# Optimization experiments

Hardware: AMD Instinct MI355X
Metric: run time of the kernel (lower is better)

The kernel has to match this reference:

```python
import jax, jax.numpy as jnp
import numpy as np

ORDER = 1024
U_SIZE = 128
Y_SIZE = 128
N_STEPS = 32768


def setup_inputs() -> dict:
    key = jax.random.key(0)
    k0, k1, k2, k3, k4 = jax.random.split(key, 5)
    inp = jax.random.normal(k0, (N_STEPS, U_SIZE), dtype=jnp.float32)
    # A scaled to spectral radius ~0.9 so the 32k-step recurrence is stable.
    A_w = jax.random.normal(k1, (ORDER, ORDER), dtype=jnp.float32) * (0.9 / np.sqrt(ORDER))
    B_w = jax.random.normal(k2, (ORDER, U_SIZE), dtype=jnp.float32) / np.sqrt(U_SIZE)
    C_w = jax.random.normal(k3, (Y_SIZE, ORDER), dtype=jnp.float32) / np.sqrt(ORDER)
    D_w = jax.random.normal(k4, (Y_SIZE, U_SIZE), dtype=jnp.float32) / np.sqrt(U_SIZE)
    return {"inp": inp, "A_w": A_w, "B_w": B_w, "C_w": C_w, "D_w": D_w}


def reference(inp, A_w, B_w, C_w, D_w):
    u_size = B_w.shape[1]
    order = A_w.shape[0]
    # Faithful to torch: input.reshape(u_size, -1), then column t is u at step t.
    us = inp.reshape(u_size, -1).T  # (N, u_size)
    x0 = jnp.zeros((order,), dtype=inp.dtype)

    def step(x, u):
        y = C_w @ x + D_w @ u          # (y_size,)
        x_next = A_w @ x + B_w @ u     # (order,)
        return x_next, y

    _, ys = jax.lax.scan(step, x0, us)
    return ys  # (N, y_size)
```

## Files before the change

### kernel.cpp

```cpp
#include <hip/hip_runtime.h>
#include <hip/hip_bf16.h>


#define NSTEPS 32768
#define LTRUNC 64
#define NDBLK  (LTRUNC + 1)
#define KTOT   (NDBLK * 128)
#define SPLITK 2

typedef __attribute__((ext_vector_type(8))) short short8;
typedef __attribute__((ext_vector_type(4))) float f32x4;
typedef __hip_bfloat16 bf16;

#define ME 1048576
#define O_AHR 0
#define O_ALR (1*ME)
#define O_AHC (2*ME)
#define O_ALC (3*ME)
#define O_XPH (4*ME)
#define O_XPL (5*ME)
#define O_XQH (6*ME)
#define O_XQL (7*ME)
#define O_YPH (8*ME)
#define O_YPL (9*ME)
#define O_YQH (10*ME)
#define O_YQL (11*ME)
#define O_GH  (12*ME)
#define O_GL  (14*ME)
#define O_RTH (16*ME)
#define O_RTL (O_RTH + 917504)
#define O_KBT (O_RTL + 917504)
#define O_UBF (O_KBT + 128*KTOT)

__device__ __forceinline__ void gload16(const void* g, void* l) {
  __builtin_amdgcn_global_load_lds(
      (const __attribute__((address_space(1))) void*)g,
      (__attribute__((address_space(3))) void*)l, 16, 0, 0);
}

__device__ __forceinline__ void split1(float x, bf16& h, bf16& l) {
  h = __float2bfloat16(x);
  l = __float2bfloat16(x - __bfloat162float(h));
}

__global__ __launch_bounds__(256) void prep(
    const float* __restrict__ inp, const float* __restrict__ Aw,
    const float* __restrict__ Bw, const float* __restrict__ Cw,
    const float* __restrict__ Dw, bf16* __restrict__ W, float* __restrict__ out)
{
  __shared__ float buf[128 * 65];
  const int tid = threadIdx.x;
  const int bid = blockIdx.x;

  if (bid < 512) {
    const int t0 = bid << 6;
#pragma unroll
    for (int i = 0; i < 32; ++i) {
      const int e = i * 256 + tid, sl = e >> 6, tl = e & 63;
      buf[sl * 65 + tl] = inp[(size_t)sl * NSTEPS + t0 + tl];
    }
    __syncthreads();
    bf16* Ubf = W + O_UBF;
#pragma unroll
    for (int i = 0; i < 32; ++i) {
      const int e = i * 256 + tid, tl = e >> 7, sl = e & 127;
      Ubf[(size_t)(LTRUNC + t0 + tl) * 128 + sl] = __float2bfloat16(buf[sl * 65 + tl]);
    }
  } else if (bid < 768) {
    const int base = (bid - 512) * 4096;
    bf16* hi = W + O_AHR; bf16* lo = W + O_ALR;
#pragma unroll
    for (int i = 0; i < 4; ++i) {
      const int e = base + i * 1024 + tid * 4;
      const float4 v = *reinterpret_cast<const float4*>(Aw + e);
      const float vv[4] = {v.x, v.y, v.z, v.w};
#pragma unroll
      for (int j = 0; j < 4; ++j) { bf16 h, l; split1(vv[j], h, l); hi[e+j] = h; lo[e+j] = l; }
    }
  } else if (bid < 1024) {
    const int idx = bid - 768;
    const int r0 = (idx >> 4) << 6, c0 = (idx & 15) << 6;
#pragma unroll
    for (int i = 0; i < 16; ++i) {
      const int e = i * 256 + tid, rl = e >> 6, cl = e & 63;
      buf[rl * 65 + cl] = Aw[(size_t)(r0 + rl) * 1024 + c0 + cl];
    }
    __syncthreads();
    bf16* hi = W + O_AHC; bf16* lo = W + O_ALC;
#pragma unroll
    for (int i = 0; i < 16; ++i) {
      const int e = i * 256 + tid, cl = e >> 6, rl = e & 63;
      bf16 h, l; split1(buf[rl * 65 + cl], h, l);
      hi[(size_t)(c0 + cl) * 1024 + r0 + rl] = h;
      lo[(size_t)(c0 + cl) * 1024 + r0 + rl] = l;
    }
  } else if (bid < 1056) {
    const int base = (bid - 1024) * 4096;
    bf16* hi = W + O_GH; bf16* lo = W + O_GL;
#pragma unroll
    for (int i = 0; i < 4; ++i) {
      const int e = base + i * 1024 + tid * 4;
      const float4 v = *reinterpret_cast<const float4*>(Cw + e);
      const float vv[4] = {v.x, v.y, v.z, v.w};
#pragma unroll
      for (int j = 0; j < 4; ++j) { bf16 h, l; split1(vv[j], h, l); hi[e+j] = h; lo[e+j] = l; }
    }
  } else if (bid < 1088) {
    const int idx = bid - 1056;
    const int r0 = (idx >> 1) << 6, c0 = (idx & 1) << 6;
#pragma unroll
    for (int i = 0; i < 16; ++i) {
      const int e = i * 256 + tid, rl = e >> 6, cl = e & 63;
      buf[rl * 65 + cl] = Bw[(size_t)(r0 + rl) * 128 + c0 + cl];
    }
    __syncthreads();
    bf16* hi = W + O_RTH; bf16* lo = W + O_RTL;
#pragma unroll
    for (int i = 0; i < 16; ++i) {
      const int e = i * 256 + tid, cl = e >> 6, rl = e & 63;
      bf16 h, l; split1(buf[rl * 65 + cl], h, l);
      hi[(size_t)(c0 + cl) * 1024 + r0 + rl] = h;
      lo[(size_t)(c0 + cl) * 1024 + r0 + rl] = l;
    }
  } else if (bid < 1092) {
    bf16* kb = W + O_KBT;
    const int e0 = (bid - 1088) * 4096 + tid * 16;
#pragma unroll
    for (int j = 0; j < 16; ++j) {
      const int e = e0 + j, r = e >> 7, s = e & 127;
      kb[(size_t)r * KTOT + s] = __float2bfloat16(Dw[e]);
    }
  } else if (bid < 1094) {
    bf16* Ubf = W + O_UBF;
    const int e = ((bid - 1092) * 256 + tid) * 16;
    short8 z = {0,0,0,0,0,0,0,0};
    *reinterpret_cast<short8*>(Ubf + e) = z;
    *reinterpret_cast<short8*>(Ubf + e + 8) = z;
  } else {
    float4* o4 = reinterpret_cast<float4*>(out);
    const int base = (bid - 1094) * 4096;
    const float4 z = {0.f, 0.f, 0.f, 0.f};
#pragma unroll
    for (int i = 0; i < 16; ++i) o4[base + i * 256 + tid] = z;
  }
}

struct Job { int ah, al, bh, bl, oh, ol, oth, otl, mt, nt, dbase; };
__device__ const Job JOBS[15] = {
  {O_AHR,O_ALR,O_AHC,O_ALC, O_XPH,O_XPL, O_YPH,O_YPL, 8,8,-1},
  {O_GH, O_GL, O_AHC,O_ALC, O_GH+131072,O_GL+131072, -1,-1, 1,8,-1},
  {O_XPH,O_XPL,O_YPH,O_YPL, O_XQH,O_XQL, O_YQH,O_YQL, 8,8,-1},
  {O_GH, O_GL, O_YPH,O_YPL, O_GH+262144,O_GL+262144, -1,-1, 2,8,-1},
  {O_XQH,O_XQL,O_YQH,O_YQL, O_XPH,O_XPL, O_YPH,O_YPL, 8,8,-1},
  {O_GH, O_GL, O_YQH,O_YQL, O_GH+524288,O_GL+524288, -1,-1, 4,8,-1},
  {O_XPH,O_XPL,O_YPH,O_YPL, O_XQH,O_XQL, O_YQH,O_YQL, 8,8,-1},
  {O_GH, O_GL, O_YPH,O_YPL, O_GH+1048576,O_GL+1048576, -1,-1, 8,8,-1},
  {O_XQH,O_XQL,O_YQH,O_YQL, O_XPH,O_XPL, -1,-1, 8,8,-1},
  {O_RTH,O_RTL,O_XQH,O_XQL, O_RTH+131072,O_RTL+131072, -1,-1, 1,8,-1},
  {O_GH,O_GL, O_RTH,        O_RTL,        O_KBT,0, -1,-1, 16,1, 1},
  {O_RTH,O_RTL,O_XPH,O_XPL, O_RTH+262144,O_RTL+262144, -1,-1, 2,8,-1},
  {O_GH,O_GL, O_RTH+131072, O_RTL+131072, O_KBT,0, -1,-1, 16,1, 17},
  {O_GH,O_GL, O_RTH+262144, O_RTL+262144, O_KBT,0, -1,-1, 16,1, 33},
  {O_GH,O_GL, O_RTH+393216, O_RTL+393216, O_KBT,0, -1,-1, 16,1, 49},
};
__device__ const int LVL[8] = {0,2,4,6,8,11,13,15};

__global__ __launch_bounds__(256) void chain_lvl(bf16* __restrict__ ws, int lvl)
{
  __shared__ __align__(16) char smem[131072];
  const int tid = threadIdx.x, lane = tid & 63, wave = tid >> 6;
  const int wm = wave & 1, wn = wave >> 1, l15 = lane & 15, lk = lane >> 4;
  const int srow = tid >> 3, sc8 = (tid & 7) << 3;
  const int g8 = (((tid & 7) ^ (srow & 7)) << 3);
  const int ca0 = ((lk ^ (l15 & 7)) << 3);
  const int ca1 = (((4 + lk) ^ (l15 & 7)) << 3);

  int idx = blockIdx.x;
  int j = LVL[lvl];
  const int je = LVL[lvl + 1];
  while (j < je && idx >= JOBS[j].mt * JOBS[j].nt) { idx -= JOBS[j].mt * JOBS[j].nt; ++j; }
  if (j >= je) return;
  const Job job = JOBS[j];
  const int my = idx / job.nt, nx = idx - my * job.nt;
  const int m0 = my << 7, n0 = nx << 7;
  const bf16* Ah = ws + job.ah; const bf16* Al = ws + job.al;
  const bf16* Bh = ws + job.bh; const bf16* Bl = ws + job.bl;
  f32x4 acc[4][4] = {};

  auto stage = [&](int ks, int buf) {
    char* base = smem + buf * 65536;
    const int k0 = ks << 6;
#pragma unroll
    for (int p = 0; p < 4; ++p) {
      const int row = (p << 5) + srow;
      const int loff = row * 128 + (sc8 << 1);
      const size_t aoff = (size_t)(m0 + row) * 1024 + k0 + g8;
      const size_t boff = (size_t)(n0 + row) * 1024 + k0 + g8;
      gload16(Ah + aoff, base + loff);
      gload16(Al + aoff, base + 16384 + loff);
      gload16(Bh + boff, base + 32768 + loff);
      gload16(Bl + boff, base + 49152 + loff);
    }
  };

  stage(0, 0);
  for (int ks = 0; ks < 16; ++ks) {
    if (ks + 1 < 16) {
      stage(ks + 1, (ks + 1) & 1);
      asm volatile("s_waitcnt vmcnt(16)" ::: "memory");
    } else {
      asm volatile("s_waitcnt vmcnt(0)" ::: "memory");
    }
    __builtin_amdgcn_s_barrier();
    __builtin_amdgcn_sched_barrier(0);
    {
      char* base = smem + (ks & 1) * 65536;
      const bf16* pAh = (const bf16*)(base);
      const bf16* pAl = (const bf16*)(base + 16384);
      const bf16* pBh = (const bf16*)(base + 32768);
      const bf16* pBl = (const bf16*)(base + 49152);
#pragma unroll
      for (int kh = 0; kh < 2; ++kh) {
        const int cb = kh ? ca1 : ca0;
        short8 ah[4], al[4], bh[4], bl[4];
#pragma unroll
        for (int mi = 0; mi < 4; ++mi) {
          const int r = ((wm << 6) + (mi << 4) + l15) * 64 + cb;
          ah[mi] = *reinterpret_cast<const short8*>(pAh + r);
          al[mi] = *reinterpret_cast<const short8*>(pAl + r);
        }
#pragma unroll
        for (int ni = 0; ni < 4; ++ni) {
          const int r = ((wn << 6) + (ni << 4) + l15) * 64 + cb;
          bh[ni] = *reinterpret_cast<const short8*>(pBh + r);
          bl[ni] = *reinterpret_cast<const short8*>(pBl + r);
        }
#pragma unroll
        for (int mi = 0; mi < 4; ++mi)
#pragma unroll
          for (int ni = 0; ni < 4; ++ni) {
            acc[mi][ni] = __builtin_amdgcn_mfma_f32_16x16x32_bf16(ah[mi], bh[ni], acc[mi][ni], 0, 0, 0);
            acc[mi][ni] = __builtin_amdgcn_mfma_f32_16x16x32_bf16(ah[mi], bl[ni], acc[mi][ni], 0, 0, 0);
            acc[mi][ni] = __builtin_amdgcn_mfma_f32_16x16x32_bf16(al[mi], bh[ni], acc[mi][ni], 0, 0, 0);
          }
      }
    }
    __builtin_amdgcn_sched_barrier(0);
    __builtin_amdgcn_s_barrier();
  }

  if (job.dbase >= 0) {
    bf16* kb = ws + job.oh;
    const int d = job.dbase + my;
#pragma unroll
    for (int mi = 0; mi < 4; ++mi)
#pragma unroll
      for (int ni = 0; ni < 4; ++ni) {
        const int cl = (wn << 6) + (ni << 4) + l15;
#pragma unroll
        for (int rg = 0; rg < 4; ++rg) {
          const int rl = (wm << 6) + (mi << 4) + (lk << 2) + rg;
          bf16 h, l; split1(acc[mi][ni][rg], h, l);
          kb[(size_t)rl * KTOT + (size_t)d * 128 + cl] = h;
        }
      }
  } else {
    bf16* oh = ws + job.oh; bf16* ol = ws + job.ol;
#pragma unroll
    for (int mi = 0; mi < 4; ++mi)
#pragma unroll
      for (int ni = 0; ni < 4; ++ni) {
        const int cl = (wn << 6) + (ni << 4) + l15;
#pragma unroll
        for (int rg = 0; rg < 4; ++rg) {
          const int rl = (wm << 6) + (mi << 4) + (lk << 2) + rg;
          bf16 h, l; split1(acc[mi][ni][rg], h, l);
          oh[(size_t)(m0 + rl) * 1024 + n0 + cl] = h;
          ol[(size_t)(m0 + rl) * 1024 + n0 + cl] = l;
        }
      }
    if (job.oth >= 0) {
      float* tT = (float*)smem;
      __syncthreads();
#pragma unroll
      for (int mi = 0; mi < 4; ++mi)
#pragma unroll
        for (int ni = 0; ni < 4; ++ni) {
          const int cl = (wn << 6) + (ni << 4) + l15;
#pragma unroll
          for (int rg = 0; rg < 4; ++rg) {
            const int rl = (wm << 6) + (mi << 4) + (lk << 2) + rg;
            tT[rl * 129 + cl] = acc[mi][ni][rg];
          }
        }
      __syncthreads();
      bf16* yh = ws + job.oth; bf16* yl = ws + job.otl;
#pragma unroll
      for (int i = 0; i < 64; ++i) {
        const int e = i * 256 + tid, yr = e >> 7, yc = e & 127;
        bf16 h, l; split1(tT[yc * 129 + yr], h, l);
        yh[(size_t)(n0 + yr) * 1024 + m0 + yc] = h;
        yl[(size_t)(n0 + yr) * 1024 + m0 + yc] = l;
      }
    }
  }
}

__global__ __launch_bounds__(256) void conv_mfma(
    const bf16* __restrict__ Ubf, const bf16* __restrict__ Kbt, float* __restrict__ out)
{
  __shared__ __align__(16) bf16 As[2][128 * 64];
  __shared__ __align__(16) bf16 Bs[2][128 * 64];
  const int tid = threadIdx.x;
  const int t0 = blockIdx.x << 7;
  const int lane = tid & 63, wave = tid >> 6;
  const int wm = wave & 1, wn = wave >> 1;
  const int l15 = lane & 15, lk = lane >> 4;
  const int srow = tid >> 3, sc8 = (tid & 7) << 3;
  const int g8 = (((tid & 7) ^ (srow & 7)) << 3);
  const int ca0 = ((lk ^ (l15 & 7)) << 3);
  const int ca1 = (((4 + lk) ^ (l15 & 7)) << 3);
  const int ntot = KTOT / 64;
  const int sb = (blockIdx.y * ntot) / SPLITK;
  const int se = ((blockIdx.y + 1) * ntot) / SPLITK;
  f32x4 acc[4][4] = {};

  auto stage = [&](int it, int buf) {
    const int kk0 = it << 6;
    const int d = kk0 >> 7, s0 = kk0 & 127;
    const bf16* srcA = Ubf + (size_t)(LTRUNC + t0 - d) * 128 + s0;
    const bf16* srcB = Kbt + kk0;
#pragma unroll
    for (int p = 0; p < 4; ++p) {
      const int row = (p << 5) + srow;
      gload16(srcA + (size_t)row * 128 + g8, &As[buf][row * 64 + sc8]);
      gload16(srcB + (size_t)row * KTOT + g8, &Bs[buf][row * 64 + sc8]);
    }
  };

  stage(sb, 0);
  int cur = 0;
  for (int it = sb; it < se; ++it) {
    if (it + 1 < se) {
      stage(it + 1, cur ^ 1);
      asm volatile("s_waitcnt vmcnt(8)" ::: "memory");
    } else {
      asm volatile("s_waitcnt vmcnt(0)" ::: "memory");
    }
    __builtin_amdgcn_s_barrier();
    __builtin_amdgcn_sched_barrier(0);
#pragma unroll
    for (int kh = 0; kh < 2; ++kh) {
      const int cb = kh ? ca1 : ca0;
      short8 a[4], b[4];
#pragma unroll
      for (int mi = 0; mi < 4; ++mi)
        a[mi] = *reinterpret_cast<const short8*>(&As[cur][((wm << 6) + (mi << 4) + l15) * 64 + cb]);
#pragma unroll
      for (int ni = 0; ni < 4; ++ni)
        b[ni] = *reinterpret_cast<const short8*>(&Bs[cur][((wn << 6) + (ni << 4) + l15) * 64 + cb]);
#pragma unroll
      for (int mi = 0; mi < 4; ++mi)
#pragma unroll
        for (int ni = 0; ni < 4; ++ni)
          acc[mi][ni] = __builtin_amdgcn_mfma_f32_16x16x32_bf16(a[mi], b[ni], acc[mi][ni], 0, 0, 0);
    }
    __builtin_amdgcn_sched_barrier(0);
    __builtin_amdgcn_s_barrier();
    cur ^= 1;
  }
#pragma unroll
  for (int mi = 0; mi < 4; ++mi)
#pragma unroll
    for (int ni = 0; ni < 4; ++ni) {
      const int rcol = (wn << 6) + (ni << 4) + l15;
#pragma unroll
      for (int rg = 0; rg < 4; ++rg) {
        const int t = t0 + (wm << 6) + (mi << 4) + (lk << 2) + rg;
        atomicAdd(out + (size_t)t * 128 + rcol, acc[mi][ni][rg]);
      }
    }
}

extern "C" void kernel_launch(void* const* d_in, const int* in_sizes, int n_in,
                              void* d_out, int out_size, void* d_ws, size_t ws_size,
                              hipStream_t stream)
{
  const float* inp = (const float*)d_in[0];
  const float* Aw  = (const float*)d_in[1];
  const float* Bw  = (const float*)d_in[2];
  const float* Cw  = (const float*)d_in[3];
  const float* Dw  = (const float*)d_in[4];
  float* out = (float*)d_out;
  (void)in_sizes; (void)n_in; (void)out_size; (void)ws_size;

  bf16* W = (bf16*)d_ws;

  prep<<<1350, 256, 0, stream>>>(inp, Aw, Bw, Cw, Dw, W, out);

  const int lvl_wgs[7] = {72, 80, 96, 128, 88, 32, 32};
  for (int lvl = 0; lvl < 7; ++lvl)
    chain_lvl<<<lvl_wgs[lvl], 256, 0, stream>>>(W, lvl);

  conv_mfma<<<dim3(NSTEPS / 128, SPLITK), 256, 0, stream>>>(W + O_UBF, W + O_KBT, out);
}
```

Baseline: 327.8 us.

## Keep U window resident in LDS for conv and use bf16-only kernel-tap GEMMs

The convolution kernel now loads the whole 128+d input window once into a swizzled LDS buffer and streams only the Kbt tiles. Each tap is taken as a row-shifted view of that resident window, so the per-iteration reload of overlapping U rows is gone. The split-K boundaries are hardcoded to the d ranges. Separately, the Markov-parameter jobs (dbase>=0) now use a single bf16 product instead of the three-term hi/lo split and write only a hi bf16 value. This cuts MFMA work and loads for those jobs but lowers their precision. LDS use grows to 72KB, which may limit occupancy.

```diff
diff --git a/kernel.cpp b/kernel.cpp
--- a/kernel.cpp
+++ b/kernel.cpp
@@ -187,6 +187,68 @@
   const bf16* Bh = ws + job.bh; const bf16* Bl = ws + job.bl;
   f32x4 acc[4][4] = {};
 
+  if (job.dbase >= 0) {
+    auto stageK = [&](int ks, int buf) {
+      char* base = smem + buf * 32768;
+      const int k0 = ks << 6;
+#pragma unroll
+      for (int p = 0; p < 4; ++p) {
+        const int row = (p << 5) + srow;
+        const int loff = row * 128 + (sc8 << 1);
+        gload16(Ah + (size_t)(m0 + row) * 1024 + k0 + g8, base + loff);
+        gload16(Bh + (size_t)(n0 + row) * 1024 + k0 + g8, base + 16384 + loff);
+      }
+    };
+    stageK(0, 0);
+    for (int ks = 0; ks < 16; ++ks) {
+      if (ks + 1 < 16) {
+        stageK(ks + 1, (ks + 1) & 1);
+        asm volatile("s_waitcnt vmcnt(8)" ::: "memory");
+      } else {
+        asm volatile("s_waitcnt vmcnt(0)" ::: "memory");
+      }
+      __builtin_amdgcn_s_barrier();
+      __builtin_amdgcn_sched_barrier(0);
+      {
+        char* base = smem + (ks & 1) * 32768;
+        const bf16* pAh = (const bf16*)(base);
+        const bf16* pBh = (const bf16*)(base + 16384);
+#pragma unroll
+        for (int kh = 0; kh < 2; ++kh) {
+          const int cb = kh ? ca1 : ca0;
+          short8 ah[4], bh[4];
+#pragma unroll
+          for (int mi = 0; mi < 4; ++mi)
+            ah[mi] = *reinterpret_cast<const short8*>(pAh + ((wm << 6) + (mi << 4) + l15) * 64 + cb);
+#pragma unroll
+          for (int ni = 0; ni < 4; ++ni)
+            bh[ni] = *reinterpret_cast<const short8*>(pBh + ((wn << 6) + (ni << 4) + l15) * 64 + cb);
+#pragma unroll
+          for (int mi = 0; mi < 4; ++mi)
+#pragma unroll
+            for (int ni = 0; ni < 4; ++ni)
+              acc[mi][ni] = __builtin_amdgcn_mfma_f32_16x16x32_bf16(ah[mi], bh[ni], acc[mi][ni], 0, 0, 0);
+        }
+      }
+      __builtin_amdgcn_sched_barrier(0);
+      __builtin_amdgcn_s_barrier();
+    }
+    bf16* kb = ws + job.oh;
+    const int d = job.dbase + my;
+#pragma unroll
+    for (int mi = 0; mi < 4; ++mi)
+#pragma unroll
+      for (int ni = 0; ni < 4; ++ni) {
+        const int cl = (wn << 6) + (ni << 4) + l15;
+#pragma unroll
+        for (int rg = 0; rg < 4; ++rg) {
+          const int rl = (wm << 6) + (mi << 4) + (lk << 2) + rg;
+          kb[(size_t)rl * KTOT + (size_t)d * 128 + cl] = __float2bfloat16(acc[mi][ni][rg]);
+        }
+      }
+    return;
+  }
+
   auto stage = [&](int ks, int buf) {
     char* base = smem + buf * 65536;
     const int k0 = ks << 6;
@@ -249,22 +311,7 @@
     __builtin_amdgcn_s_barrier();
   }
 
-  if (job.dbase >= 0) {
-    bf16* kb = ws + job.oh;
-    const int d = job.dbase + my;
-#pragma unroll
-    for (int mi = 0; mi < 4; ++mi)
-#pragma unroll
-      for (int ni = 0; ni < 4; ++ni) {
-        const int cl = (wn << 6) + (ni << 4) + l15;
-#pragma unroll
-        for (int rg = 0; rg < 4; ++rg) {
-          const int rl = (wm << 6) + (mi << 4) + (lk << 2) + rg;
-          bf16 h, l; split1(acc[mi][ni][rg], h, l);
-          kb[(size_t)rl * KTOT + (size_t)d * 128 + cl] = h;
-        }
-      }
-  } else {
+  {
     bf16* oh = ws + job.oh; bf16* ol = ws + job.ol;
 #pragma unroll
     for (int mi = 0; mi < 4; ++mi)
@@ -309,10 +356,10 @@
 __global__ __launch_bounds__(256) void conv_mfma(
     const bf16* __restrict__ Ubf, const bf16* __restrict__ Kbt, float* __restrict__ out)
 {
-  __shared__ __align__(16) bf16 As[2][128 * 64];
-  __shared__ __align__(16) bf16 Bs[2][128 * 64];
+  __shared__ __align__(16) char smem[73728];
   const int tid = threadIdx.x;
   const int t0 = blockIdx.x << 7;
+  const int y = blockIdx.y;
   const int lane = tid & 63, wave = tid >> 6;
   const int wm = wave & 1, wn = wave >> 1;
   const int l15 = lane & 15, lk = lane >> 4;
@@ -320,50 +367,65 @@
   const int g8 = (((tid & 7) ^ (srow & 7)) << 3);
   const int ca0 = ((lk ^ (l15 & 7)) << 3);
   const int ca1 = (((4 + lk) ^ (l15 & 7)) << 3);
-  const int ntot = KTOT / 64;
-  const int sb = (blockIdx.y * ntot) / SPLITK;
-  const int se = ((blockIdx.y + 1) * ntot) / SPLITK;
+  const int d_hi = y ? LTRUNC : 32;
+  const int sb = y ? 66 : 0, se = y ? 130 : 66;
+  bf16* U = (bf16*)smem;
+  bf16* Bs0 = (bf16*)(smem + 40960);
+  bf16* Bs1 = (bf16*)(smem + 57344);
   f32x4 acc[4][4] = {};
 
-  auto stage = [&](int it, int buf) {
+  const long u0 = (long)LTRUNC + t0 - d_hi;
+#pragma unroll
+  for (int i = 0; i < 10; ++i) {
+    const int idx = i * 256 + tid;
+    const int r = idx >> 4, c = idx & 15;
+    gload16(Ubf + (size_t)(u0 + r) * 128 + ((c ^ (r & 15)) << 3), smem + idx * 16);
+  }
+
+  auto stageB = [&](int it, bf16* Bbuf) {
     const int kk0 = it << 6;
-    const int d = kk0 >> 7, s0 = kk0 & 127;
-    const bf16* srcA = Ubf + (size_t)(LTRUNC + t0 - d) * 128 + s0;
-    const bf16* srcB = Kbt + kk0;
 #pragma unroll
     for (int p = 0; p < 4; ++p) {
       const int row = (p << 5) + srow;
-      gload16(srcA + (size_t)row * 128 + g8, &As[buf][row * 64 + sc8]);
-      gload16(srcB + (size_t)row * KTOT + g8, &Bs[buf][row * 64 + sc8]);
+      gload16(Kbt + (size_t)row * KTOT + kk0 + g8, Bbuf + row * 64 + sc8);
     }
   };
 
-  stage(sb, 0);
+  stageB(sb, Bs0);
   int cur = 0;
   for (int it = sb; it < se; ++it) {
     if (it + 1 < se) {
-      stage(it + 1, cur ^ 1);
-      asm volatile("s_waitcnt vmcnt(8)" ::: "memory");
+      stageB(it + 1, cur ? Bs0 : Bs1);
+      asm volatile("s_waitcnt vmcnt(4)" ::: "memory");
     } else {
       asm volatile("s_waitcnt vmcnt(0)" ::: "memory");
     }
     __builtin_amdgcn_s_barrier();
     __builtin_amdgcn_sched_barrier(0);
-#pragma unroll
-    for (int kh = 0; kh < 2; ++kh) {
-      const int cb = kh ? ca1 : ca0;
-      short8 a[4], b[4];
-#pragma unroll
-      for (int mi = 0; mi < 4; ++mi)
-        a[mi] = *reinterpret_cast<const short8*>(&As[cur][((wm << 6) + (mi << 4) + l15) * 64 + cb]);
-#pragma unroll
-      for (int ni = 0; ni < 4; ++ni)
-        b[ni] = *reinterpret_cast<const short8*>(&Bs[cur][((wn << 6) + (ni << 4) + l15) * 64 + cb]);
-#pragma unroll
-      for (int mi = 0; mi < 4; ++mi)
+    {
+      const bf16* Bcur = cur ? Bs1 : Bs0;
+      const int d = it >> 1;
+      const int dhd = d_hi - d;
+      const int cbase = (it & 1) << 3;
+#pragma unroll
+      for (int kh = 0; kh < 2; ++kh) {
+        short8 a[4], b[4];
+#pragma unroll
+        for (int mi = 0; mi < 4; ++mi) {
+          const int row = dhd + (wm << 6) + (mi << 4) + l15;
+          const int ch = (cbase + (kh << 2) + lk) ^ (row & 15);
+          a[mi] = *reinterpret_cast<const short8*>(U + row * 128 + (ch << 3));
+        }
+        const int cb = kh ? ca1 : ca0;
 #pragma unroll
         for (int ni = 0; ni < 4; ++ni)
-          acc[mi][ni] = __builtin_amdgcn_mfma_f32_16x16x32_bf16(a[mi], b[ni], acc[mi][ni], 0, 0, 0);
+          b[ni] = *reinterpret_cast<const short8*>(Bcur + ((wn << 6) + (ni << 4) + l15) * 64 + cb);
+#pragma unroll
+        for (int mi = 0; mi < 4; ++mi)
+#pragma unroll
+          for (int ni = 0; ni < 4; ++ni)
+            acc[mi][ni] = __builtin_amdgcn_mfma_f32_16x16x32_bf16(a[mi], b[ni], acc[mi][ni], 0, 0, 0);
+      }
     }
     __builtin_amdgcn_sched_barrier(0);
     __builtin_amdgcn_s_barrier();
```

After: 294.8 us. 10.1% less time.
